# Kernel tuning notes

Measured on AMD Instinct MI355X. Metric: run time of the kernel, lower is better.

Reference implementation:

```python
import jax, jax.numpy as jnp
import numpy as np

B, T, E, QKV, H = 2, 2048, 1024, 1024, 16
DH = QKV // H
R_LAYER = 2

def rmsnorm(x):
    eps = jnp.finfo(x.dtype).eps
    return x * jax.lax.rsqrt(jnp.mean(x * x, axis=-1, keepdims=True) + eps)

def w_norm(w, n):
    # scale whole matrix so its (unbiased) std matches n**-0.5
    std = jnp.std(w, ddof=1)
    return w * (n ** -0.5 / (std + 1e-8))

def rotary(x, cos, sin):
    d = x.shape[-1] // 2
    x1, x2 = x[..., :d], x[..., d:]
    return jnp.concatenate([x1 * cos + x2 * sin, -x1 * sin + x2 * cos], axis=-1)

def w_split(w):
    w_qkv = w[:3 * QKV]                               # (3*QKV, E)
    w_sw = w[3 * QKV:5 * QKV].reshape(2 * E, QKV)     # (2*E, QKV)
    w_out = w[5 * QKV:]                               # (E, E)
    return w_qkv, w_sw, w_out

def aft(x, w_qkv):
    qkv = rmsnorm(x) @ w_qkv.T                        # (B,T,3*QKV)
    q, k, v = jnp.split(qkv, 3, axis=-1)
    q, k = rmsnorm(q), rmsnorm(k)
    wexp = jnp.exp(k)
    kv_c = jnp.cumsum(wexp * v, axis=1)
    w_c = jnp.cumsum(wexp, axis=1)
    y = jax.nn.sigmoid(q) * kv_c / (w_c + 1e-6)
    return x, y

def tea(x, cos, sin, w_qkv):
    qkv = (rmsnorm(x) @ w_qkv.T).reshape(B, T, H, 3 * DH)
    q, k, v = jnp.split(qkv, 3, axis=-1)              # each (B,T,H,DH)
    q, k = rotary(q, cos, sin), rotary(k, cos, sin)
    q, k = rmsnorm(q), rmsnorm(k)
    q = q.transpose(0, 2, 1, 3)                       # (B,H,T,DH)
    k = k.transpose(0, 2, 1, 3)
    v = v.transpose(0, 2, 1, 3)
    scores = jnp.einsum('bhqd,bhkd->bhqk', q, k) * DH ** -0.5
    mask = jnp.tril(jnp.ones((T, T), dtype=bool))
    scores = jnp.where(mask, scores, -jnp.inf)
    att = jax.nn.softmax(scores, axis=-1)
    y = jnp.einsum('bhqk,bhkd->bhqd', att, v)
    return x, y.transpose(0, 2, 1, 3).reshape(B, T, QKV)

def swiglu(x, y, w_sw, w_out, ret_oa=True):
    uv = y @ w_sw.T                                   # (B,T,2*E)
    u, v = jnp.split(uv, 2, axis=-1)
    out = x + (u * jax.nn.silu(v)) @ w_out.T
    if not ret_oa:
        return out
    o = rmsnorm(u.reshape(B * T, -1))
    a = v.reshape(B * T, -1)
    oa = jax.nn.softmax((o.T @ a) * E ** -0.5, axis=-1)  # (E,E)
    return out, oa

def setup_inputs():
    key = jax.random.key(0)
    k1, k2 = jax.random.split(key)
    x = jax.random.normal(k1, (B, T, E), dtype=jnp.float32)
    s = 3 ** 0.5 * E ** -0.5
    w = jax.random.uniform(k2, (5 * QKV + E, E), dtype=jnp.float32, minval=-s, maxval=s)
    half = DH // 2
    inv_freq = 1.0 / (10000.0 ** (jnp.arange(half, dtype=jnp.float32) / half))
    freqs = jnp.outer(jnp.arange(T, dtype=jnp.float32), inv_freq)  # (T, half)
    cos = jnp.cos(freqs)[:, None, :]                  # (T,1,half) broadcasts over (B,T,H,half)
    sin = jnp.sin(freqs)[:, None, :]
    return {"x": x, "w": w, "cos": cos, "sin": sin}

def reference(x, w, cos, sin):
    for i in range(R_LAYER):
        w_qkv, w_sw, w_out = w_split(w)
        w_qkv = w_norm(w_qkv, E)
        w_sw = w_norm(w_sw, QKV)
        w_out = w_norm(w_out, E)
        if (i + 1) % 4 == 0:
            x, y = tea(x, cos, sin, w_qkv)
        else:
            x, y = aft(x, w_qkv)
        x, oa = swiglu(x, y, w_sw, w_out, ret_oa=True)
        # RetentionMechanism.forward: hypernetwork weight mixing
        wT = w_norm(w @ oa, 5 * QKV + E)
        w = wT * jax.nn.silu(w) + w
    w_qkv, w_sw, w_out = w_split(w)                   # note: no w_norm on final split (matches source)
    x, y = tea(x, cos, sin, w_qkv)
    return swiglu(x, y, w_sw, w_out, ret_oa=False)
```

## Files before the change

kernel.cpp:

```cpp
#include <hip/hip_runtime.h>
#include <hip/hip_bf16.h>
#include <math.h>

#define TPB 256

constexpr int Bc = 2, Tc = 2048, Ec = 1024, QKVc = 1024, Hc = 16, DHc = 64;
constexpr long BT = (long)Bc * Tc;
constexpr int WR = 5 * QKVc + Ec;
constexpr float F32_EPS = 1.1920928955078125e-07f;
constexpr int NCH = 64, CHL = Tc / NCH;

typedef __attribute__((ext_vector_type(8))) short short8;
typedef __attribute__((ext_vector_type(4))) float f32x4;

__device__ __forceinline__ unsigned short f2bu(float f) {
    union { __hip_bfloat16 h; unsigned short u; } c; c.h = __float2bfloat16(f); return c.u;
}
__device__ __forceinline__ float bu2f(unsigned short u) {
    union { __hip_bfloat16 h; unsigned short u; } c; c.u = u; return __bfloat162float(c.h);
}
__device__ __forceinline__ float ldval(const float* p) { return *p; }
__device__ __forceinline__ float ldval(const unsigned short* p) { return bu2f(*p); }

__device__ __forceinline__ void gload_lds16(const void* g, void* l) {
    __builtin_amdgcn_global_load_lds((const __attribute__((address_space(1))) void*)g,
                                     (__attribute__((address_space(3))) void*)l, 16, 0, 0);
}

__global__ void k_std_partial3(const float* __restrict__ w, float* __restrict__ out) {
    __shared__ float ls[TPB], lss[TPB];
    int seg = blockIdx.y;
    long base = (seg == 0) ? 0L : (seg == 1 ? 3072L * 1024 : 5120L * 1024);
    long n    = (seg == 0) ? 3072L * 1024 : (seg == 1 ? 2048L * 1024 : 1024L * 1024);
    const float* p = w + base;
    float s = 0.f, ss = 0.f;
    for (long i = (long)blockIdx.x * TPB + threadIdx.x; i < n; i += 256L * TPB) {
        float v = p[i]; s += v; ss += v * v;
    }
    ls[threadIdx.x] = s; lss[threadIdx.x] = ss; __syncthreads();
    for (int o = 128; o > 0; o >>= 1) {
        if (threadIdx.x < o) { ls[threadIdx.x] += ls[threadIdx.x + o]; lss[threadIdx.x] += lss[threadIdx.x + o]; }
        __syncthreads();
    }
    if (threadIdx.x == 0) { out[seg * 512 + blockIdx.x] = ls[0]; out[seg * 512 + 256 + blockIdx.x] = lss[0]; }
}

__global__ void k_std_final3(const float* __restrict__ part, float* __restrict__ scales) {
    __shared__ float ls[TPB], lss[TPB];
    for (int seg = 0; seg < 3; ++seg) {
        ls[threadIdx.x] = part[seg * 512 + threadIdx.x];
        lss[threadIdx.x] = part[seg * 512 + 256 + threadIdx.x];
        __syncthreads();
        for (int o = 128; o > 0; o >>= 1) {
            if (threadIdx.x < o) { ls[threadIdx.x] += ls[threadIdx.x + o]; lss[threadIdx.x] += lss[threadIdx.x + o]; }
            __syncthreads();
        }
        if (threadIdx.x == 0) {
            float n = (seg == 0) ? 3145728.0f : (seg == 1 ? 2097152.0f : 1048576.0f);
            float var = (lss[0] - ls[0] * ls[0] / n) / (n - 1.0f);
            scales[seg] = 0.03125f / (sqrtf(fmaxf(var, 0.0f)) + 1e-8f);
        }
        __syncthreads();
    }
}

__global__ void k_std_partial(const float* __restrict__ p, long n, float* __restrict__ out) {
    __shared__ float ls[TPB], lss[TPB];
    float s = 0.f, ss = 0.f;
    for (long i = (long)blockIdx.x * TPB + threadIdx.x; i < n; i += (long)gridDim.x * TPB) {
        float v = p[i]; s += v; ss += v * v;
    }
    ls[threadIdx.x] = s; lss[threadIdx.x] = ss; __syncthreads();
    for (int o = 128; o > 0; o >>= 1) {
        if (threadIdx.x < o) { ls[threadIdx.x] += ls[threadIdx.x + o]; lss[threadIdx.x] += lss[threadIdx.x + o]; }
        __syncthreads();
    }
    if (threadIdx.x == 0) { out[blockIdx.x] = ls[0]; out[gridDim.x + blockIdx.x] = lss[0]; }
}

__global__ void k_std_final(const float* __restrict__ part, float n, float rs, float* __restrict__ scale) {
    __shared__ float ls[TPB], lss[TPB];
    ls[threadIdx.x] = part[threadIdx.x];
    lss[threadIdx.x] = part[TPB + threadIdx.x];
    __syncthreads();
    for (int o = 128; o > 0; o >>= 1) {
        if (threadIdx.x < o) { ls[threadIdx.x] += ls[threadIdx.x + o]; lss[threadIdx.x] += lss[threadIdx.x + o]; }
        __syncthreads();
    }
    if (threadIdx.x == 0) {
        float var = (lss[0] - ls[0] * ls[0] / n) / (n - 1.0f);
        scale[0] = rs / (sqrtf(fmaxf(var, 0.0f)) + 1e-8f);
    }
}

__global__ void k_rms_qk(float* __restrict__ qkv) {
    __shared__ float red[TPB];
    int bid = blockIdx.x;
    long row = bid >> 1; int half = bid & 1;
    float* p = qkv + row * 3072 + half * 1024;
    float4 v = *(const float4*)(p + threadIdx.x * 4);
    float ss = v.x * v.x + v.y * v.y + v.z * v.z + v.w * v.w;
    red[threadIdx.x] = ss; __syncthreads();
    for (int o = 128; o > 0; o >>= 1) {
        if (threadIdx.x < o) red[threadIdx.x] += red[threadIdx.x + o];
        __syncthreads();
    }
    float sc = rsqrtf(red[0] / 1024.0f + F32_EPS);
    float4 o4; o4.x = v.x * sc; o4.y = v.y * sc; o4.z = v.z * sc; o4.w = v.w * sc;
    *(float4*)(p + threadIdx.x * 4) = o4;
}

__global__ void k_rms1024b(const float* __restrict__ in, unsigned short* __restrict__ out, long ldin, long ldout) {
    __shared__ float red[TPB];
    long row = blockIdx.x;
    float4 v = *(const float4*)(in + row * ldin + threadIdx.x * 4);
    float ss = v.x * v.x + v.y * v.y + v.z * v.z + v.w * v.w;
    red[threadIdx.x] = ss; __syncthreads();
    for (int o = 128; o > 0; o >>= 1) {
        if (threadIdx.x < o) red[threadIdx.x] += red[threadIdx.x + o];
        __syncthreads();
    }
    float sc = rsqrtf(red[0] / 1024.0f + F32_EPS);
    ushort4 o4; o4.x = f2bu(v.x * sc); o4.y = f2bu(v.y * sc); o4.z = f2bu(v.z * sc); o4.w = f2bu(v.w * sc);
    *(ushort4*)(out + row * ldout + threadIdx.x * 4) = o4;
}

__global__ void k_cast_bf16(const float* __restrict__ in, unsigned short* __restrict__ out, long n4) {
    long i = (long)blockIdx.x * TPB + threadIdx.x;
    if (i >= n4) return;
    float4 v = *(const float4*)(in + i * 4);
    ushort4 o; o.x = f2bu(v.x); o.y = f2bu(v.y); o.z = f2bu(v.z); o.w = f2bu(v.w);
    *(ushort4*)(out + i * 4) = o;
}

template<typename TI>
__global__ void k_tcast(const TI* __restrict__ in, long ldi, long sIn,
                        unsigned short* __restrict__ out, long ldo, long sOut,
                        const float* __restrict__ rowscale) {
    __shared__ float tile[64][65];
    const TI* ip = in + (long)blockIdx.z * sIn;
    unsigned short* op = out + (long)blockIdx.z * sOut;
    int r0 = blockIdx.y * 64, c0 = blockIdx.x * 64;
    int tid = threadIdx.x;
    int rr = tid >> 4, cc = (tid & 15) * 4;
    #pragma unroll
    for (int u = 0; u < 4; ++u) {
        int r = rr + u * 16;
        float sc = rowscale ? rowscale[r0 + r] : 1.0f;
        #pragma unroll
        for (int j = 0; j < 4; ++j)
            tile[r][cc + j] = ldval(ip + (long)(r0 + r) * ldi + c0 + cc + j) * sc;
    }
    __syncthreads();
    #pragma unroll
    for (int u = 0; u < 4; ++u) {
        int c = rr + u * 16;
        ushort4 o;
        o.x = f2bu(tile[cc + 0][c]); o.y = f2bu(tile[cc + 1][c]);
        o.z = f2bu(tile[cc + 2][c]); o.w = f2bu(tile[cc + 3][c]);
        *(ushort4*)(op + (long)(c0 + c) * ldo + r0 + cc) = o;
    }
}

__global__ void k_tcast2(const float* __restrict__ uv, const float* __restrict__ uscale,
                         unsigned short* __restrict__ t1, unsigned short* __restrict__ t2) {
    __shared__ float tile[64][65];
    int z = blockIdx.z;
    const float* ip = uv + (z ? 1024 : 0);
    unsigned short* op = z ? t2 : t1;
    int r0 = blockIdx.y * 64, c0 = blockIdx.x * 64;
    int tid = threadIdx.x;
    int rr = tid >> 4, cc = (tid & 15) * 4;
    #pragma unroll
    for (int u = 0; u < 4; ++u) {
        int r = rr + u * 16;
        float sc = z ? 1.0f : uscale[r0 + r];
        #pragma unroll
        for (int j = 0; j < 4; ++j)
            tile[r][cc + j] = ip[(long)(r0 + r) * 2048 + c0 + cc + j] * sc;
    }
    __syncthreads();
    #pragma unroll
    for (int u = 0; u < 4; ++u) {
        int c = rr + u * 16;
        ushort4 o;
        o.x = f2bu(tile[cc + 0][c]); o.y = f2bu(tile[cc + 1][c]);
        o.z = f2bu(tile[cc + 2][c]); o.w = f2bu(tile[cc + 3][c]);
        *(ushort4*)(op + (long)(c0 + c) * 4096 + r0 + cc) = o;
    }
}

template<int WGM, int WGN, int WRITE_BF16>
__global__ __launch_bounds__(256)
void k_bgemm(int K,
             const unsigned short* __restrict__ A, int lda, long sA,
             const unsigned short* __restrict__ B, int ldb, long sB,
             void* __restrict__ C, int ldc, long sCi, long sSplit, int nsplit,
             const float* __restrict__ scale_ptr, float fscale,
             const float* __restrict__ addp, int ldadd) {
    constexpr int TM = WGM * 64, TN = WGN * 64;
    __shared__ unsigned short Asl[TM * 32];
    __shared__ unsigned short Bsl[TN * 32];
    int bz = blockIdx.z;
    int batch = bz, sp = 0;
    if (nsplit > 1) { batch = bz / nsplit; sp = bz - batch * nsplit; }
    int m0 = blockIdx.y * TM, n0 = blockIdx.x * TN;
    const unsigned short* Ap = A + (long)batch * sA + (long)sp * K;
    const unsigned short* Bp = B + (long)batch * sB + (long)sp * K;
    int tid = threadIdx.x, lane = tid & 63, wave = tid >> 6;
    int wr = wave / WGN, wc = wave % WGN;
    f32x4 acc[4][4] = {};
    constexpr int CAW = TM / 64;
    constexpr int CBW = TN / 64;
    for (int k0 = 0; k0 < K; k0 += 32) {
        #pragma unroll
        for (int c = 0; c < CAW; ++c) {
            int bu = (wave * CAW + c) * 64;
            int uidx = bu + lane;
            int r = uidx >> 2, slot = uidx & 3;
            int gu = slot ^ ((r >> 1) & 3);
            gload_lds16(Ap + (long)(m0 + r) * lda + k0 + gu * 8, Asl + bu * 8);
        }
        #pragma unroll
        for (int c = 0; c < CBW; ++c) {
            int bu = (wave * CBW + c) * 64;
            int uidx = bu + lane;
            int r = uidx >> 2, slot = uidx & 3;
            int gu = slot ^ ((r >> 1) & 3);
            gload_lds16(Bp + (long)(n0 + r) * ldb + k0 + gu * 8, Bsl + bu * 8);
        }
        __syncthreads();
        short8 av[4], bv[4];
        #pragma unroll
        for (int m = 0; m < 4; ++m) {
            int r = wr * 64 + m * 16 + (lane & 15);
            int slot = (lane >> 4) ^ ((r >> 1) & 3);
            av[m] = *(const short8*)(Asl + r * 32 + slot * 8);
        }
        #pragma unroll
        for (int n = 0; n < 4; ++n) {
            int r = wc * 64 + n * 16 + (lane & 15);
            int slot = (lane >> 4) ^ ((r >> 1) & 3);
            bv[n] = *(const short8*)(Bsl + r * 32 + slot * 8);
        }
        #pragma unroll
        for (int m = 0; m < 4; ++m)
            #pragma unroll
            for (int n = 0; n < 4; ++n)
                acc[m][n] = __builtin_amdgcn_mfma_f32_16x16x32_bf16(av[m], bv[n], acc[m][n], 0, 0, 0);
        __syncthreads();
    }
    float s = fscale * (scale_ptr ? scale_ptr[0] : 1.0f);
    long cbase = (long)batch * sCi + (long)sp * sSplit;
    int row0 = m0 + wr * 64, col0 = n0 + wc * 64 + (lane & 15);
    int rbase = (lane >> 4) * 4;
    #pragma unroll
    for (int m = 0; m < 4; ++m)
        #pragma unroll
        for (int i = 0; i < 4; ++i) {
            long row = row0 + m * 16 + rbase + i;
            #pragma unroll
            for (int n = 0; n < 4; ++n) {
                long col = col0 + n * 16;
                float v = acc[m][n][i] * s;
                if (addp) v += addp[row * (long)ldadd + col];
                long idx = cbase + row * ldc + col;
                if (WRITE_BF16) ((unsigned short*)C)[idx] = f2bu(v);
                else ((float*)C)[idx] = v;
            }
        }
}

__global__ __launch_bounds__(256)
void k_flash_split(const unsigned short* __restrict__ hq, const unsigned short* __restrict__ hk,
                   const unsigned short* __restrict__ hvT,
                   float* __restrict__ opart, float* __restrict__ mpart, float* __restrict__ lpart) {
    __shared__ unsigned short P_lds[4][32 * 72];
    int lane = threadIdx.x & 63, wave = threadIdx.x >> 6;
    unsigned short* P = P_lds[wave];
    int g = lane >> 4, c = lane & 15;
    unsigned bid = blockIdx.x;
    unsigned bswz = (bid & 7) * 160 + (bid >> 3);
    unsigned gi = bswz * 4 + wave;
    unsigned bh = gi / 160, itr = gi % 160;
    int item = 159 - (int)itr;
    int strip, chunk;
    if (item < 16)      { strip = item;                 chunk = 0; }
    else if (item < 48) { strip = 16 + (item - 16) / 2; chunk = (item - 16) & 1; }
    else if (item < 96) { strip = 32 + (item - 48) / 3; chunk = (item - 48) % 3; }
    else                { strip = 48 + (item - 96) / 4; chunk = (item - 96) & 3; }
    int q0 = strip * 32;
    int nt = (q0 + 32 + 63) >> 6;
    int ti0 = chunk * 8;
    int ti1 = ti0 + 8 < nt ? ti0 + 8 : nt;
    const unsigned short* qb = hq + (long)bh * Tc * 64;
    const unsigned short* kb = hk + (long)bh * Tc * 64;
    const unsigned short* vtb = hvT + (long)bh * 64 * Tc;

    short8 qf[2][2];
    #pragma unroll
    for (int mf = 0; mf < 2; ++mf)
        #pragma unroll
        for (int ks = 0; ks < 2; ++ks)
            qf[mf][ks] = *(const short8*)(qb + (long)(q0 + mf * 16 + c) * 64 + ks * 32 + g * 8);

    f32x4 o_acc[2][4] = {};
    float m_run[2][4], lpp[2][4];
    #pragma unroll
    for (int mf = 0; mf < 2; ++mf)
        #pragma unroll
        for (int i = 0; i < 4; ++i) { m_run[mf][i] = -3.0e38f; lpp[mf][i] = 0.f; }

    for (int ti = ti0; ti < ti1; ++ti) {
        int kt = ti * 64;
        short8 vf[2][4];
        #pragma unroll
        for (int ks = 0; ks < 2; ++ks)
            #pragma unroll
            for (int df = 0; df < 4; ++df)
                vf[ks][df] = *(const short8*)(vtb + (long)(df * 16 + c) * Tc + kt + ks * 32 + g * 8);
        f32x4 s_acc[2][4] = {};
        #pragma unroll
        for (int ks = 0; ks < 2; ++ks) {
            short8 kf[4];
            #pragma unroll
            for (int nf = 0; nf < 4; ++nf)
                kf[nf] = *(const short8*)(kb + (long)(kt + nf * 16 + c) * 64 + ks * 32 + g * 8);
            #pragma unroll
            for (int mf = 0; mf < 2; ++mf)
                #pragma unroll
                for (int nf = 0; nf < 4; ++nf)
                    s_acc[mf][nf] = __builtin_amdgcn_mfma_f32_16x16x32_bf16(qf[mf][ks], kf[nf], s_acc[mf][nf], 0, 0, 0);
        }
        if (ti == nt - 1) {
            #pragma unroll
            for (int mf = 0; mf < 2; ++mf)
                #pragma unroll
                for (int nf = 0; nf < 4; ++nf)
                    #pragma unroll
                    for (int i = 0; i < 4; ++i)
                        if ((kt + nf * 16 + c) > (q0 + mf * 16 + g * 4 + i)) s_acc[mf][nf][i] = -1.0e30f;
        }
        float pm[2][4];
        #pragma unroll
        for (int mf = 0; mf < 2; ++mf)
            #pragma unroll
            for (int i = 0; i < 4; ++i)
                pm[mf][i] = fmaxf(fmaxf(s_acc[mf][0][i], s_acc[mf][1][i]),
                                  fmaxf(s_acc[mf][2][i], s_acc[mf][3][i]));
        #pragma unroll
        for (int lvl = 1; lvl <= 8; lvl <<= 1)
            #pragma unroll
            for (int mf = 0; mf < 2; ++mf)
                #pragma unroll
                for (int i = 0; i < 4; ++i)
                    pm[mf][i] = fmaxf(pm[mf][i], __shfl_xor(pm[mf][i], lvl));
        float mg = 0.f;
        #pragma unroll
        for (int mf = 0; mf < 2; ++mf)
            #pragma unroll
            for (int i = 0; i < 4; ++i) {
                pm[mf][i] *= 0.125f;
                mg = fmaxf(mg, pm[mf][i] - m_run[mf][i]);
            }
        if (__any(mg > 8.0f)) {
            #pragma unroll
            for (int mf = 0; mf < 2; ++mf)
                #pragma unroll
                for (int i = 0; i < 4; ++i) {
                    float mn = fmaxf(m_run[mf][i], pm[mf][i]);
                    float corr = __expf(m_run[mf][i] - mn);
                    m_run[mf][i] = mn;
                    lpp[mf][i] *= corr;
                    #pragma unroll
                    for (int df = 0; df < 4; ++df) o_acc[mf][df][i] *= corr;
                }
        }
        #pragma unroll
        for (int mf = 0; mf < 2; ++mf)
            #pragma unroll
            for (int nf = 0; nf < 4; ++nf)
                #pragma unroll
                for (int i = 0; i < 4; ++i) {
                    float p = __expf(fmaf(s_acc[mf][nf][i], 0.125f, -m_run[mf][i]));
                    P[(mf * 16 + g * 4 + i) * 72 + nf * 16 + c] = f2bu(p);
                    lpp[mf][i] += p;
                }
        #pragma unroll
        for (int ks = 0; ks < 2; ++ks) {
            short8 pa[2];
            #pragma unroll
            for (int mf = 0; mf < 2; ++mf)
                pa[mf] = *(const short8*)(P + (mf * 16 + c) * 72 + ks * 32 + g * 8);
            #pragma unroll
            for (int mf = 0; mf < 2; ++mf)
                #pragma unroll
                for (int df = 0; df < 4; ++df)
                    o_acc[mf][df] = __builtin_amdgcn_mfma_f32_16x16x32_bf16(pa[mf], vf[ks][df], o_acc[mf][df], 0, 0, 0);
        }
    }
    #pragma unroll
    for (int lvl = 1; lvl <= 8; lvl <<= 1)
        #pragma unroll
        for (int mf = 0; mf < 2; ++mf)
            #pragma unroll
            for (int i = 0; i < 4; ++i)
                lpp[mf][i] += __shfl_xor(lpp[mf][i], lvl);
    long pbase = (long)(bh * 160 + item);
    #pragma unroll
    for (int mf = 0; mf < 2; ++mf)
        #pragma unroll
        for (int i = 0; i < 4; ++i) {
            int row_l = mf * 16 + g * 4 + i;
            #pragma unroll
            for (int df = 0; df < 4; ++df)
                opart[pbase * 2048 + row_l * 64 + df * 16 + c] = o_acc[mf][df][i];
            if (c == 0) {
                mpart[pbase * 32 + row_l] = m_run[mf][i];
                lpart[pbase * 32 + row_l] = lpp[mf][i];
            }
        }
}

__global__ __launch_bounds__(256)
void k_flash_merge(const float* __restrict__ opart, const float* __restrict__ mpart,
                   const float* __restrict__ lpart, unsigned short* __restrict__ yout) {
    int bs = blockIdx.x;
    int bh = bs >> 6, strip = bs & 63;
    int b = bh >> 4, h = bh & 15;
    int np, base;
    if (strip < 16)      { np = 1; base = strip; }
    else if (strip < 32) { np = 2; base = 16 + (strip - 16) * 2; }
    else if (strip < 48) { np = 3; base = 48 + (strip - 32) * 3; }
    else                 { np = 4; base = 96 + (strip - 48) * 4; }
    long p0 = (long)(bh * 160 + base);
    int tid = threadIdx.x;
    int r = tid >> 3, c0 = (tid & 7) * 8;
    float M = -3.0e38f;
    for (int p = 0; p < np; ++p) M = fmaxf(M, mpart[(p0 + p) * 32 + r]);
    float L = 0.f;
    float acc[8] = {};
    for (int p = 0; p < np; ++p) {
        float sc = __expf(mpart[(p0 + p) * 32 + r] - M);
        L += lpart[(p0 + p) * 32 + r] * sc;
        const float* op = opart + (p0 + p) * 2048 + r * 64 + c0;
        #pragma unroll
        for (int j = 0; j < 8; ++j) acc[j] += op[j] * sc;
    }
    float inv = 1.0f / L;
    long row = (long)b * Tc + strip * 32 + r;
    unsigned short* yp = yout + row * 1024 + h * 64 + c0;
    ushort4 o1, o2;
    o1.x = f2bu(acc[0] * inv); o1.y = f2bu(acc[1] * inv); o1.z = f2bu(acc[2] * inv); o1.w = f2bu(acc[3] * inv);
    o2.x = f2bu(acc[4] * inv); o2.y = f2bu(acc[5] * inv); o2.z = f2bu(acc[6] * inv); o2.w = f2bu(acc[7] * inv);
    *(ushort4*)yp = o1;
    *(ushort4*)(yp + 4) = o2;
}

__global__ void k_aft_p1(const float* __restrict__ qkv, float* __restrict__ cw, float* __restrict__ cs) {
    int id = blockIdx.x * TPB + threadIdx.x;
    int bc = id & 2047, ch = id >> 11;
    int b = bc >> 10, c = bc & 1023;
    const float* base = qkv + ((long)(b * Tc + ch * CHL)) * 3072 + c;
    float sw = 0.f, sv = 0.f;
    for (int i = 0; i < CHL; ++i) {
        float k = base[1024], v = base[2048];
        float e = __expf(k);
        sw += e; sv += e * v;
        base += 3072;
    }
    cw[ch * 2048 + bc] = sw; cs[ch * 2048 + bc] = sv;
}

__global__ void k_aft_p3(const float* __restrict__ qkv, const float* __restrict__ cw,
                         const float* __restrict__ cs, unsigned short* __restrict__ y) {
    int id = blockIdx.x * TPB + threadIdx.x;
    int bc = id & 2047, ch = id >> 11;
    int b = bc >> 10, c = bc & 1023;
    float aw = 0.f, av = 0.f;
    for (int cc = 0; cc < ch; ++cc) { aw += cw[cc * 2048 + bc]; av += cs[cc * 2048 + bc]; }
    long t0 = (long)b * Tc + ch * CHL;
    const float* base = qkv + t0 * 3072 + c;
    unsigned short* yp = y + t0 * 1024 + c;
    for (int i = 0; i < CHL; ++i) {
        float q = base[0], k = base[1024], v = base[2048];
        float e = __expf(k);
        av += e * v; aw += e;
        float sig = 1.0f / (1.0f + __expf(-q));
        yp[0] = f2bu(sig * av / (aw + 1e-6f));
        base += 3072; yp += 1024;
    }
}

__global__ void k_silu_rms(const float* __restrict__ uv, unsigned short* __restrict__ g,
                           float* __restrict__ rs) {
    __shared__ float red[TPB];
    long row = blockIdx.x;
    const float* up = uv + row * 2048;
    float4 u = *(const float4*)(up + threadIdx.x * 4);
    float4 v = *(const float4*)(up + 1024 + threadIdx.x * 4);
    ushort4 o;
    o.x = f2bu(u.x * v.x / (1.f + __expf(-v.x)));
    o.y = f2bu(u.y * v.y / (1.f + __expf(-v.y)));
    o.z = f2bu(u.z * v.z / (1.f + __expf(-v.z)));
    o.w = f2bu(u.w * v.w / (1.f + __expf(-v.w)));
    *(ushort4*)(g + row * 1024 + threadIdx.x * 4) = o;
    red[threadIdx.x] = u.x * u.x + u.y * u.y + u.z * u.z + u.w * u.w;
    __syncthreads();
    for (int off = 128; off > 0; off >>= 1) {
        if (threadIdx.x < off) red[threadIdx.x] += red[threadIdx.x + off];
        __syncthreads();
    }
    if (threadIdx.x == 0) rs[row] = rsqrtf(red[0] / 1024.0f + F32_EPS);
}

__global__ void k_silu_gate(const float* __restrict__ uv, unsigned short* __restrict__ g, long n4) {
    long i = (long)blockIdx.x * TPB + threadIdx.x;
    if (i >= n4) return;
    long r = i >> 8, c4 = i & 255;
    float4 u = *(const float4*)(uv + r * 2048 + c4 * 4);
    float4 v = *(const float4*)(uv + r * 2048 + 1024 + c4 * 4);
    ushort4 o;
    o.x = f2bu(u.x * v.x / (1.f + __expf(-v.x)));
    o.y = f2bu(u.y * v.y / (1.f + __expf(-v.y)));
    o.z = f2bu(u.z * v.z / (1.f + __expf(-v.z)));
    o.w = f2bu(u.w * v.w / (1.f + __expf(-v.w)));
    *(ushort4*)(g + r * 1024 + c4 * 4) = o;
}

__global__ void k_wupdate(float* __restrict__ wout, const float* __restrict__ win,
                          const float* __restrict__ p, const float* __restrict__ scale,
                          unsigned short* __restrict__ wb, long n4) {
    long i = (long)blockIdx.x * TPB + threadIdx.x;
    if (i >= n4) return;
    float s = scale[0];
    float4 wv = *(const float4*)(win + i * 4);
    float4 pv = *(const float4*)(p + i * 4);
    float4 o;
    o.x = pv.x * s * (wv.x / (1.f + __expf(-wv.x))) + wv.x;
    o.y = pv.y * s * (wv.y / (1.f + __expf(-wv.y))) + wv.y;
    o.z = pv.z * s * (wv.z / (1.f + __expf(-wv.z))) + wv.z;
    o.w = pv.w * s * (wv.w / (1.f + __expf(-wv.w))) + wv.w;
    *(float4*)(wout + i * 4) = o;
    ushort4 ob; ob.x = f2bu(o.x); ob.y = f2bu(o.y); ob.z = f2bu(o.z); ob.w = f2bu(o.w);
    *(ushort4*)(wb + i * 4) = ob;
}

__global__ void k_softmax4(const float* __restrict__ parts, float* __restrict__ outb, float fscale) {
    __shared__ float red[TPB];
    __shared__ float rowbuf[1024];
    long row = blockIdx.x;
    const float* p0 = parts + row * 1024;
    for (int c = threadIdx.x; c < 1024; c += TPB) {
        float v = p0[c] + p0[c + 1048576] + p0[c + 2097152] + p0[c + 3145728];
        rowbuf[c] = v * fscale;
    }
    __syncthreads();
    float m = -3.0e38f;
    for (int c = threadIdx.x; c < 1024; c += TPB) m = fmaxf(m, rowbuf[c]);
    red[threadIdx.x] = m; __syncthreads();
    for (int o = 128; o > 0; o >>= 1) {
        if (threadIdx.x < o) red[threadIdx.x] = fmaxf(red[threadIdx.x], red[threadIdx.x + o]);
        __syncthreads();
    }
    m = red[0]; __syncthreads();
    float sum = 0.f;
    for (int c = threadIdx.x; c < 1024; c += TPB) sum += __expf(rowbuf[c] - m);
    red[threadIdx.x] = sum; __syncthreads();
    for (int o = 128; o > 0; o >>= 1) {
        if (threadIdx.x < o) red[threadIdx.x] += red[threadIdx.x + o];
        __syncthreads();
    }
    float inv = 1.0f / red[0];
    for (int c = threadIdx.x; c < 1024; c += TPB)
        outb[row * 1024 + c] = __expf(rowbuf[c] - m) * inv;
}

__global__ void k_rot_split(const float* __restrict__ qkvp, const float* __restrict__ cosp,
                            const float* __restrict__ sinp, unsigned short* __restrict__ hq,
                            unsigned short* __restrict__ hk, unsigned short* __restrict__ hv) {
    __shared__ float row[3072];
    __shared__ float cs[32], sn[32];
    int bt = blockIdx.x;
    int b = bt >> 11, t = bt & 2047;
    const float* src = qkvp + (long)bt * 3072;
    #pragma unroll
    for (int u = 0; u < 3; ++u) {
        int idx = threadIdx.x + u * 256;
        *(float4*)&row[idx * 4] = *(const float4*)(src + idx * 4);
    }
    if (threadIdx.x < 32) { cs[threadIdx.x] = cosp[t * 32 + threadIdx.x]; sn[threadIdx.x] = sinp[t * 32 + threadIdx.x]; }
    __syncthreads();
    int h = threadIdx.x >> 4, li = threadIdx.x & 15;
    int base = h * 192;
    long obase = ((long)(b * Hc + h) * Tc + t) * 64 + li * 4;
    {
        float r[4]; float ss = 0.f;
        #pragma unroll
        for (int j = 0; j < 4; ++j) {
            int d = li * 4 + j;
            float val = (d < 32) ? (row[base + d] * cs[d] + row[base + d + 32] * sn[d])
                                 : (-row[base + d - 32] * sn[d - 32] + row[base + d] * cs[d - 32]);
            r[j] = val; ss += val * val;
        }
        ss += __shfl_xor(ss, 1); ss += __shfl_xor(ss, 2); ss += __shfl_xor(ss, 4); ss += __shfl_xor(ss, 8);
        float sc = rsqrtf(ss / 64.0f + F32_EPS);
        ushort4 o; o.x = f2bu(r[0] * sc); o.y = f2bu(r[1] * sc); o.z = f2bu(r[2] * sc); o.w = f2bu(r[3] * sc);
        *(ushort4*)(hq + obase) = o;
    }
    {
        int kb = base + 64;
        float r[4]; float ss = 0.f;
        #pragma unroll
        for (int j = 0; j < 4; ++j) {
            int d = li * 4 + j;
            float val = (d < 32) ? (row[kb + d] * cs[d] + row[kb + d + 32] * sn[d])
                                 : (-row[kb + d - 32] * sn[d - 32] + row[kb + d] * cs[d - 32]);
            r[j] = val; ss += val * val;
        }
        ss += __shfl_xor(ss, 1); ss += __shfl_xor(ss, 2); ss += __shfl_xor(ss, 4); ss += __shfl_xor(ss, 8);
        float sc = rsqrtf(ss / 64.0f + F32_EPS);
        ushort4 o; o.x = f2bu(r[0] * sc); o.y = f2bu(r[1] * sc); o.z = f2bu(r[2] * sc); o.w = f2bu(r[3] * sc);
        *(ushort4*)(hk + obase) = o;
    }
    {
        ushort4 o;
        o.x = f2bu(row[base + 128 + li * 4 + 0]); o.y = f2bu(row[base + 128 + li * 4 + 1]);
        o.z = f2bu(row[base + 128 + li * 4 + 2]); o.w = f2bu(row[base + 128 + li * 4 + 3]);
        *(ushort4*)(hv + obase) = o;
    }
}

extern "C" void kernel_launch(void* const* d_in, const int* in_sizes, int n_in,
                              void* d_out, int out_size, void* d_ws, size_t ws_size,
                              hipStream_t stream) {
    const float* x_in = (const float*)d_in[0];
    const float* w_in = (const float*)d_in[1];
    const float* cos_in = (const float*)d_in[2];
    const float* sin_in = (const float*)d_in[3];
    float* out = (float*)d_out;
    float* ws = (float*)d_ws;

    long off = 0;
    float* w_cur = ws + off;  off += (long)WR * Ec;
    float* w_tmp = ws + off;  off += (long)WR * Ec;
    float* xbuf  = ws + off;  off += BT * Ec;
    float* qkv   = ws + off;  off += BT * 3L * QKVc;
    float* oab   = ws + off;  off += (long)Ec * Ec;
    float* red   = ws + off;  off += 2048;
    float* scales= ws + off;  off += 16;
    float* uscale= ws + off;  off += 4096;
    float* chw   = ws + off;  off += 2048L * NCH;
    float* chs   = ws + off;  off += 2048L * NCH;
    float* uv    = qkv;
    float* opart = qkv;
    float* mpart = oab;
    float* lpart = oab + 5120L * 32;

    unsigned short* bp = (unsigned short*)(ws + off);
    long bo = 0;
    unsigned short* wb  = bp + bo; bo += (long)WR * Ec;
    unsigned short* xbn = bp + bo; bo += BT * Ec;
    unsigned short* ybn = bp + bo; bo += BT * Ec;
    unsigned short* gbn = bp + bo; bo += BT * Ec;
    unsigned short* t1  = bp + bo; bo += BT * Ec;
    unsigned short* t2  = bp + bo; bo += BT * Ec;
    unsigned short* t3  = bp + bo; bo += BT * Ec;
    unsigned short* t4  = bp + bo; bo += BT * Ec;

    const float rsWR = 1.0f / sqrtf(6144.0f);
    const long wsw = 3072L * 1024, wout = 5120L * 1024;

    k_cast_bf16<<<(int)(((long)WR * Ec / 4) / TPB), TPB, 0, stream>>>(w_in, wb, (long)WR * Ec / 4);

    for (int layer = 0; layer < 2; ++layer) {
        const float* wsrc = layer == 0 ? w_in : w_cur;
        const float* xsrc = layer == 0 ? x_in : xbuf;
        k_std_partial3<<<dim3(256, 3), TPB, 0, stream>>>(wsrc, red);
        k_std_final3<<<1, TPB, 0, stream>>>(red, scales);
        k_rms1024b<<<BT, TPB, 0, stream>>>(xsrc, xbn, 1024, 1024);
        k_bgemm<2, 2, 0><<<dim3(24, 32, 1), TPB, 0, stream>>>(
            1024, xbn, 1024, 0, wb, 1024, 0, qkv, 3072, 0, 0, 1, scales + 0, 1.0f, nullptr, 0);
        k_rms_qk<<<8192, TPB, 0, stream>>>(qkv);
        k_aft_p1<<<(2048 * NCH) / TPB, TPB, 0, stream>>>(qkv, chw, chs);
        k_aft_p3<<<(2048 * NCH) / TPB, TPB, 0, stream>>>(qkv, chw, chs, ybn);
        k_bgemm<2, 2, 0><<<dim3(16, 32, 1), TPB, 0, stream>>>(
            1024, ybn, 1024, 0, wb + wsw, 1024, 0, uv, 2048, 0, 0, 1, scales + 1, 1.0f, nullptr, 0);
        k_silu_rms<<<BT, TPB, 0, stream>>>(uv, gbn, uscale);
        k_tcast2<<<dim3(16, 64, 2), TPB, 0, stream>>>(uv, uscale, t1, t2);
        k_bgemm<2, 2, 0><<<dim3(8, 8, 4), TPB, 0, stream>>>(
            1024, t1, 4096, 0, t2, 4096, 0, w_tmp, 1024, 0, 1048576L, 4, nullptr, 1.0f, nullptr, 0);
        k_softmax4<<<1024, TPB, 0, stream>>>(w_tmp, oab, 0.03125f);
        k_tcast<float><<<dim3(16, 16, 1), TPB, 0, stream>>>(oab, 1024, 0, t3, 1024, 0, nullptr);
        k_bgemm<2, 2, 0><<<dim3(8, 32, 1), TPB, 0, stream>>>(
            1024, gbn, 1024, 0, wb + wout, 1024, 0, xbuf, 1024, 0, 0, 1, scales + 2, 1.0f, xsrc, 1024);
        k_bgemm<2, 2, 0><<<dim3(8, 48, 1), TPB, 0, stream>>>(
            1024, wb, 1024, 0, t3, 1024, 0, w_tmp, 1024, 0, 0, 1, nullptr, 1.0f, nullptr, 0);
        k_std_partial<<<256, TPB, 0, stream>>>(w_tmp, (long)WR * 1024, red);
        k_std_final<<<1, TPB, 0, stream>>>(red, (float)((long)WR * 1024), rsWR, scales + 3);
        k_wupdate<<<(int)(((long)WR * 1024 / 4) / TPB), TPB, 0, stream>>>(
            w_cur, wsrc, w_tmp, scales + 3, wb, (long)WR * 1024 / 4);
    }

    k_rms1024b<<<BT, TPB, 0, stream>>>(xbuf, xbn, 1024, 1024);
    k_bgemm<2, 2, 0><<<dim3(24, 32, 1), TPB, 0, stream>>>(
        1024, xbn, 1024, 0, wb, 1024, 0, qkv, 3072, 0, 0, 1, nullptr, 1.0f, nullptr, 0);
    k_rot_split<<<BT, TPB, 0, stream>>>(qkv, cos_in, sin_in, t1, t2, t3);
    k_tcast<unsigned short><<<dim3(1, 32, 32), TPB, 0, stream>>>(
        t3, 64, (long)Tc * 64, t4, 2048, (long)Tc * 64, nullptr);
    k_flash_split<<<dim3(1280), TPB, 0, stream>>>(t1, t2, t4, opart, mpart, lpart);
    k_flash_merge<<<dim3(2048), TPB, 0, stream>>>(opart, mpart, lpart, ybn);
    k_bgemm<2, 2, 0><<<dim3(16, 32, 1), TPB, 0, stream>>>(
        1024, ybn, 1024, 0, wb + wsw, 1024, 0, uv, 2048, 0, 0, 1, nullptr, 1.0f, nullptr, 0);
    k_silu_gate<<<(int)((BT * 1024 / 4) / TPB), TPB, 0, stream>>>(uv, gbn, BT * 1024 / 4);
    k_bgemm<2, 2, 0><<<dim3(8, 32, 1), TPB, 0, stream>>>(
        1024, gbn, 1024, 0, wb + wout, 1024, 0, out, 1024, 0, 0, 1, nullptr, 1.0f, xbuf, 1024);
}
```

Baseline: 868.3 us.

## Store QKV, UV and flash partials in bf16 and use DPP reductions

The QKV and UV GEMM outputs are now written as bf16 instead of fp32, and every consumer (rms_qk, AFT passes, silu kernels, tcast2, rot_split) reads bf16, which halves the intermediate memory traffic. Flash-attention partial outputs are also stored in bf16. Separately, the 16-lane shuffle reductions in the flash and rotary kernels are replaced with DPP-based max/sum helpers. The cost is lower precision on these intermediates, which adds rounding error before the normalizations and the cumulative sums.

Result: faster. 829.6 us (-4.5%).

```diff
diff --git a/kernel.cpp b/kernel.cpp
--- a/kernel.cpp
+++ b/kernel.cpp
@@ -25,6 +25,28 @@
 __device__ __forceinline__ void gload_lds16(const void* g, void* l) {
     __builtin_amdgcn_global_load_lds((const __attribute__((address_space(1))) void*)g,
                                      (__attribute__((address_space(3))) void*)l, 16, 0, 0);
+}
+
+template<int CTRL>
+__device__ __forceinline__ float dppf(float x) {
+    union { float f; int i; } a, b;
+    a.f = x;
+    b.i = __builtin_amdgcn_update_dpp(0, a.i, CTRL, 0xF, 0xF, true);
+    return b.f;
+}
+__device__ __forceinline__ float max16(float v) {
+    v = fmaxf(v, dppf<0xB1>(v));
+    v = fmaxf(v, dppf<0x4E>(v));
+    v = fmaxf(v, dppf<0x124>(v));
+    v = fmaxf(v, dppf<0x128>(v));
+    return v;
+}
+__device__ __forceinline__ float sum16(float v) {
+    v += dppf<0xB1>(v);
+    v += dppf<0x4E>(v);
+    v += dppf<0x124>(v);
+    v += dppf<0x128>(v);
+    return v;
 }
 
 __global__ void k_std_partial3(const float* __restrict__ w, float* __restrict__ out) {
@@ -93,21 +115,22 @@
     }
 }
 
-__global__ void k_rms_qk(float* __restrict__ qkv) {
+__global__ void k_rms_qk(unsigned short* __restrict__ qkv) {
     __shared__ float red[TPB];
     int bid = blockIdx.x;
     long row = bid >> 1; int half = bid & 1;
-    float* p = qkv + row * 3072 + half * 1024;
-    float4 v = *(const float4*)(p + threadIdx.x * 4);
-    float ss = v.x * v.x + v.y * v.y + v.z * v.z + v.w * v.w;
-    red[threadIdx.x] = ss; __syncthreads();
+    unsigned short* p = qkv + row * 3072 + half * 1024;
+    ushort4 v = *(const ushort4*)(p + threadIdx.x * 4);
+    float f0 = bu2f(v.x), f1 = bu2f(v.y), f2 = bu2f(v.z), f3 = bu2f(v.w);
+    red[threadIdx.x] = f0 * f0 + f1 * f1 + f2 * f2 + f3 * f3;
+    __syncthreads();
     for (int o = 128; o > 0; o >>= 1) {
         if (threadIdx.x < o) red[threadIdx.x] += red[threadIdx.x + o];
         __syncthreads();
     }
     float sc = rsqrtf(red[0] / 1024.0f + F32_EPS);
-    float4 o4; o4.x = v.x * sc; o4.y = v.y * sc; o4.z = v.z * sc; o4.w = v.w * sc;
-    *(float4*)(p + threadIdx.x * 4) = o4;
+    ushort4 o4; o4.x = f2bu(f0 * sc); o4.y = f2bu(f1 * sc); o4.z = f2bu(f2 * sc); o4.w = f2bu(f3 * sc);
+    *(ushort4*)(p + threadIdx.x * 4) = o4;
 }
 
 __global__ void k_rms1024b(const float* __restrict__ in, unsigned short* __restrict__ out, long ldin, long ldout) {
@@ -162,11 +185,11 @@
     }
 }
 
-__global__ void k_tcast2(const float* __restrict__ uv, const float* __restrict__ uscale,
+__global__ void k_tcast2(const unsigned short* __restrict__ uv, const float* __restrict__ uscale,
                          unsigned short* __restrict__ t1, unsigned short* __restrict__ t2) {
     __shared__ float tile[64][65];
     int z = blockIdx.z;
-    const float* ip = uv + (z ? 1024 : 0);
+    const unsigned short* ip = uv + (z ? 1024 : 0);
     unsigned short* op = z ? t2 : t1;
     int r0 = blockIdx.y * 64, c0 = blockIdx.x * 64;
     int tid = threadIdx.x;
@@ -175,9 +198,9 @@
     for (int u = 0; u < 4; ++u) {
         int r = rr + u * 16;
         float sc = z ? 1.0f : uscale[r0 + r];
-        #pragma unroll
-        for (int j = 0; j < 4; ++j)
-            tile[r][cc + j] = ip[(long)(r0 + r) * 2048 + c0 + cc + j] * sc;
+        ushort4 v = *(const ushort4*)(ip + (long)(r0 + r) * 2048 + c0 + cc);
+        tile[r][cc + 0] = bu2f(v.x) * sc; tile[r][cc + 1] = bu2f(v.y) * sc;
+        tile[r][cc + 2] = bu2f(v.z) * sc; tile[r][cc + 3] = bu2f(v.w) * sc;
     }
     __syncthreads();
     #pragma unroll
@@ -274,7 +297,7 @@
 __global__ __launch_bounds__(256)
 void k_flash_split(const unsigned short* __restrict__ hq, const unsigned short* __restrict__ hk,
                    const unsigned short* __restrict__ hvT,
-                   float* __restrict__ opart, float* __restrict__ mpart, float* __restrict__ lpart) {
+                   unsigned short* __restrict__ opart, float* __restrict__ mpart, float* __restrict__ lpart) {
     __shared__ unsigned short P_lds[4][32 * 72];
     int lane = threadIdx.x & 63, wave = threadIdx.x >> 6;
     unsigned short* P = P_lds[wave];
@@ -346,15 +369,8 @@
         for (int mf = 0; mf < 2; ++mf)
             #pragma unroll
             for (int i = 0; i < 4; ++i)
-                pm[mf][i] = fmaxf(fmaxf(s_acc[mf][0][i], s_acc[mf][1][i]),
-                                  fmaxf(s_acc[mf][2][i], s_acc[mf][3][i]));
-        #pragma unroll
-        for (int lvl = 1; lvl <= 8; lvl <<= 1)
-            #pragma unroll
-            for (int mf = 0; mf < 2; ++mf)
-                #pragma unroll
-                for (int i = 0; i < 4; ++i)
-                    pm[mf][i] = fmaxf(pm[mf][i], __shfl_xor(pm[mf][i], lvl));
+                pm[mf][i] = max16(fmaxf(fmaxf(s_acc[mf][0][i], s_acc[mf][1][i]),
+                                        fmaxf(s_acc[mf][2][i], s_acc[mf][3][i])));
         float mg = 0.f;
         #pragma unroll
         for (int mf = 0; mf < 2; ++mf)
@@ -400,12 +416,10 @@
         }
     }
     #pragma unroll
-    for (int lvl = 1; lvl <= 8; lvl <<= 1)
-        #pragma unroll
-        for (int mf = 0; mf < 2; ++mf)
-            #pragma unroll
-            for (int i = 0; i < 4; ++i)
-                lpp[mf][i] += __shfl_xor(lpp[mf][i], lvl);
+    for (int mf = 0; mf < 2; ++mf)
+        #pragma unroll
+        for (int i = 0; i < 4; ++i)
+            lpp[mf][i] = sum16(lpp[mf][i]);
     long pbase = (long)(bh * 160 + item);
     #pragma unroll
     for (int mf = 0; mf < 2; ++mf)
@@ -414,7 +428,7 @@
             int row_l = mf * 16 + g * 4 + i;
             #pragma unroll
             for (int df = 0; df < 4; ++df)
-                opart[pbase * 2048 + row_l * 64 + df * 16 + c] = o_acc[mf][df][i];
+                opart[pbase * 2048 + row_l * 64 + df * 16 + c] = f2bu(o_acc[mf][df][i]);
             if (c == 0) {
                 mpart[pbase * 32 + row_l] = m_run[mf][i];
                 lpart[pbase * 32 + row_l] = lpp[mf][i];
@@ -423,7 +437,7 @@
 }
 
 __global__ __launch_bounds__(256)
-void k_flash_merge(const float* __restrict__ opart, const float* __restrict__ mpart,
+void k_flash_merge(const unsigned short* __restrict__ opart, const float* __restrict__ mpart,
                    const float* __restrict__ lpart, unsigned short* __restrict__ yout) {
     int bs = blockIdx.x;
     int bh = bs >> 6, strip = bs & 63;
@@ -443,9 +457,13 @@
     for (int p = 0; p < np; ++p) {
         float sc = __expf(mpart[(p0 + p) * 32 + r] - M);
         L += lpart[(p0 + p) * 32 + r] * sc;
-        const float* op = opart + (p0 + p) * 2048 + r * 64 + c0;
-        #pragma unroll
-        for (int j = 0; j < 8; ++j) acc[j] += op[j] * sc;
+        const unsigned short* op = opart + (p0 + p) * 2048 + r * 64 + c0;
+        ushort4 a = *(const ushort4*)op;
+        ushort4 bq = *(const ushort4*)(op + 4);
+        acc[0] += bu2f(a.x) * sc; acc[1] += bu2f(a.y) * sc;
+        acc[2] += bu2f(a.z) * sc; acc[3] += bu2f(a.w) * sc;
+        acc[4] += bu2f(bq.x) * sc; acc[5] += bu2f(bq.y) * sc;
+        acc[6] += bu2f(bq.z) * sc; acc[7] += bu2f(bq.w) * sc;
     }
     float inv = 1.0f / L;
     long row = (long)b * Tc + strip * 32 + r;
@@ -457,14 +475,14 @@
     *(ushort4*)(yp + 4) = o2;
 }
 
-__global__ void k_aft_p1(const float* __restrict__ qkv, float* __restrict__ cw, float* __restrict__ cs) {
+__global__ void k_aft_p1(const unsigned short* __restrict__ qkv, float* __restrict__ cw, float* __restrict__ cs) {
     int id = blockIdx.x * TPB + threadIdx.x;
     int bc = id & 2047, ch = id >> 11;
     int b = bc >> 10, c = bc & 1023;
-    const float* base = qkv + ((long)(b * Tc + ch * CHL)) * 3072 + c;
+    const unsigned short* base = qkv + ((long)(b * Tc + ch * CHL)) * 3072 + c;
     float sw = 0.f, sv = 0.f;
     for (int i = 0; i < CHL; ++i) {
-        float k = base[1024], v = base[2048];
+        float k = bu2f(base[1024]), v = bu2f(base[2048]);
         float e = __expf(k);
         sw += e; sv += e * v;
         base += 3072;
@@ -472,7 +490,7 @@
     cw[ch * 2048 + bc] = sw; cs[ch * 2048 + bc] = sv;
 }
 
-__global__ void k_aft_p3(const float* __restrict__ qkv, const float* __restrict__ cw,
+__global__ void k_aft_p3(const unsigned short* __restrict__ qkv, const float* __restrict__ cw,
                          const float* __restrict__ cs, unsigned short* __restrict__ y) {
     int id = blockIdx.x * TPB + threadIdx.x;
     int bc = id & 2047, ch = id >> 11;
@@ -480,10 +498,10 @@
     float aw = 0.f, av = 0.f;
     for (int cc = 0; cc < ch; ++cc) { aw += cw[cc * 2048 + bc]; av += cs[cc * 2048 + bc]; }
     long t0 = (long)b * Tc + ch * CHL;
-    const float* base = qkv + t0 * 3072 + c;
+    const unsigned short* base = qkv + t0 * 3072 + c;
     unsigned short* yp = y + t0 * 1024 + c;
     for (int i = 0; i < CHL; ++i) {
-        float q = base[0], k = base[1024], v = base[2048];
+        float q = bu2f(base[0]), k = bu2f(base[1024]), v = bu2f(base[2048]);
         float e = __expf(k);
         av += e * v; aw += e;
         float sig = 1.0f / (1.0f + __expf(-q));
@@ -492,20 +510,22 @@
     }
 }
 
-__global__ void k_silu_rms(const float* __restrict__ uv, unsigned short* __restrict__ g,
+__global__ void k_silu_rms(const unsigned short* __restrict__ uv, unsigned short* __restrict__ g,
                            float* __restrict__ rs) {
     __shared__ float red[TPB];
     long row = blockIdx.x;
-    const float* up = uv + row * 2048;
-    float4 u = *(const float4*)(up + threadIdx.x * 4);
-    float4 v = *(const float4*)(up + 1024 + threadIdx.x * 4);
+    const unsigned short* up = uv + row * 2048;
+    ushort4 u4 = *(const ushort4*)(up + threadIdx.x * 4);
+    ushort4 v4 = *(const ushort4*)(up + 1024 + threadIdx.x * 4);
+    float u0 = bu2f(u4.x), u1 = bu2f(u4.y), u2 = bu2f(u4.z), u3 = bu2f(u4.w);
+    float v0 = bu2f(v4.x), v1 = bu2f(v4.y), v2 = bu2f(v4.z), v3 = bu2f(v4.w);
     ushort4 o;
-    o.x = f2bu(u.x * v.x / (1.f + __expf(-v.x)));
-    o.y = f2bu(u.y * v.y / (1.f + __expf(-v.y)));
-    o.z = f2bu(u.z * v.z / (1.f + __expf(-v.z)));
-    o.w = f2bu(u.w * v.w / (1.f + __expf(-v.w)));
+    o.x = f2bu(u0 * v0 / (1.f + __expf(-v0)));
+    o.y = f2bu(u1 * v1 / (1.f + __expf(-v1)));
+    o.z = f2bu(u2 * v2 / (1.f + __expf(-v2)));
+    o.w = f2bu(u3 * v3 / (1.f + __expf(-v3)));
     *(ushort4*)(g + row * 1024 + threadIdx.x * 4) = o;
-    red[threadIdx.x] = u.x * u.x + u.y * u.y + u.z * u.z + u.w * u.w;
+    red[threadIdx.x] = u0 * u0 + u1 * u1 + u2 * u2 + u3 * u3;
     __syncthreads();
     for (int off = 128; off > 0; off >>= 1) {
         if (threadIdx.x < off) red[threadIdx.x] += red[threadIdx.x + off];
@@ -514,17 +534,19 @@
     if (threadIdx.x == 0) rs[row] = rsqrtf(red[0] / 1024.0f + F32_EPS);
 }
 
-__global__ void k_silu_gate(const float* __restrict__ uv, unsigned short* __restrict__ g, long n4) {
+__global__ void k_silu_gate(const unsigned short* __restrict__ uv, unsigned short* __restrict__ g, long n4) {
     long i = (long)blockIdx.x * TPB + threadIdx.x;
     if (i >= n4) return;
     long r = i >> 8, c4 = i & 255;
-    float4 u = *(const float4*)(uv + r * 2048 + c4 * 4);
-    float4 v = *(const float4*)(uv + r * 2048 + 1024 + c4 * 4);
+    ushort4 u4 = *(const ushort4*)(uv + r * 2048 + c4 * 4);
+    ushort4 v4 = *(const ushort4*)(uv + r * 2048 + 1024 + c4 * 4);
+    float u0 = bu2f(u4.x), u1 = bu2f(u4.y), u2 = bu2f(u4.z), u3 = bu2f(u4.w);
+    float v0 = bu2f(v4.x), v1 = bu2f(v4.y), v2 = bu2f(v4.z), v3 = bu2f(v4.w);
     ushort4 o;
-    o.x = f2bu(u.x * v.x / (1.f + __expf(-v.x)));
-    o.y = f2bu(u.y * v.y / (1.f + __expf(-v.y)));
-    o.z = f2bu(u.z * v.z / (1.f + __expf(-v.z)));
-    o.w = f2bu(u.w * v.w / (1.f + __expf(-v.w)));
+    o.x = f2bu(u0 * v0 / (1.f + __expf(-v0)));
+    o.y = f2bu(u1 * v1 / (1.f + __expf(-v1)));
+    o.z = f2bu(u2 * v2 / (1.f + __expf(-v2)));
+    o.w = f2bu(u3 * v3 / (1.f + __expf(-v3)));
     *(ushort4*)(g + r * 1024 + c4 * 4) = o;
 }
 
@@ -576,18 +598,20 @@
         outb[row * 1024 + c] = __expf(rowbuf[c] - m) * inv;
 }
 
-__global__ void k_rot_split(const float* __restrict__ qkvp, const float* __restrict__ cosp,
+__global__ void k_rot_split(const unsigned short* __restrict__ qkvp, const float* __restrict__ cosp,
                             const float* __restrict__ sinp, unsigned short* __restrict__ hq,
                             unsigned short* __restrict__ hk, unsigned short* __restrict__ hv) {
     __shared__ float row[3072];
     __shared__ float cs[32], sn[32];
     int bt = blockIdx.x;
     int b = bt >> 11, t = bt & 2047;
-    const float* src = qkvp + (long)bt * 3072;
+    const unsigned short* src = qkvp + (long)bt * 3072;
     #pragma unroll
     for (int u = 0; u < 3; ++u) {
         int idx = threadIdx.x + u * 256;
-        *(float4*)&row[idx * 4] = *(const float4*)(src + idx * 4);
+        ushort4 v = *(const ushort4*)(src + idx * 4);
+        row[idx * 4 + 0] = bu2f(v.x); row[idx * 4 + 1] = bu2f(v.y);
+        row[idx * 4 + 2] = bu2f(v.z); row[idx * 4 + 3] = bu2f(v.w);
     }
     if (threadIdx.x < 32) { cs[threadIdx.x] = cosp[t * 32 + threadIdx.x]; sn[threadIdx.x] = sinp[t * 32 + threadIdx.x]; }
     __syncthreads();
@@ -603,7 +627,7 @@
                                  : (-row[base + d - 32] * sn[d - 32] + row[base + d] * cs[d - 32]);
             r[j] = val; ss += val * val;
         }
-        ss += __shfl_xor(ss, 1); ss += __shfl_xor(ss, 2); ss += __shfl_xor(ss, 4); ss += __shfl_xor(ss, 8);
+        ss = sum16(ss);
         float sc = rsqrtf(ss / 64.0f + F32_EPS);
         ushort4 o; o.x = f2bu(r[0] * sc); o.y = f2bu(r[1] * sc); o.z = f2bu(r[2] * sc); o.w = f2bu(r[3] * sc);
         *(ushort4*)(hq + obase) = o;
@@ -618,7 +642,7 @@
                                  : (-row[kb + d - 32] * sn[d - 32] + row[kb + d] * cs[d - 32]);
             r[j] = val; ss += val * val;
         }
-        ss += __shfl_xor(ss, 1); ss += __shfl_xor(ss, 2); ss += __shfl_xor(ss, 4); ss += __shfl_xor(ss, 8);
+        ss = sum16(ss);
         float sc = rsqrtf(ss / 64.0f + F32_EPS);
         ushort4 o; o.x = f2bu(r[0] * sc); o.y = f2bu(r[1] * sc); o.z = f2bu(r[2] * sc); o.w = f2bu(r[3] * sc);
         *(ushort4*)(hk + obase) = o;
@@ -645,15 +669,16 @@
     float* w_cur = ws + off;  off += (long)WR * Ec;
     float* w_tmp = ws + off;  off += (long)WR * Ec;
     float* xbuf  = ws + off;  off += BT * Ec;
-    float* qkv   = ws + off;  off += BT * 3L * QKVc;
+    float* R     = ws + off;  off += BT * 3L * QKVc;
     float* oab   = ws + off;  off += (long)Ec * Ec;
     float* red   = ws + off;  off += 2048;
     float* scales= ws + off;  off += 16;
     float* uscale= ws + off;  off += 4096;
     float* chw   = ws + off;  off += 2048L * NCH;
     float* chs   = ws + off;  off += 2048L * NCH;
-    float* uv    = qkv;
-    float* opart = qkv;
+    unsigned short* qkvb  = (unsigned short*)R;
+    unsigned short* uvb   = qkvb + 12582912L;
+    unsigned short* opartb= qkvb;
     float* mpart = oab;
     float* lpart = oab + 5120L * 32;
 
@@ -679,15 +704,15 @@
         k_std_partial3<<<dim3(256, 3), TPB, 0, stream>>>(wsrc, red);
         k_std_final3<<<1, TPB, 0, stream>>>(red, scales);
         k_rms1024b<<<BT, TPB, 0, stream>>>(xsrc, xbn, 1024, 1024);
-        k_bgemm<2, 2, 0><<<dim3(24, 32, 1), TPB, 0, stream>>>(
-            1024, xbn, 1024, 0, wb, 1024, 0, qkv, 3072, 0, 0, 1, scales + 0, 1.0f, nullptr, 0);
-        k_rms_qk<<<8192, TPB, 0, stream>>>(qkv);
-        k_aft_p1<<<(2048 * NCH) / TPB, TPB, 0, stream>>>(qkv, chw, chs);
-        k_aft_p3<<<(2048 * NCH) / TPB, TPB, 0, stream>>>(qkv, chw, chs, ybn);
-        k_bgemm<2, 2, 0><<<dim3(16, 32, 1), TPB, 0, stream>>>(
-            1024, ybn, 1024, 0, wb + wsw, 1024, 0, uv, 2048, 0, 0, 1, scales + 1, 1.0f, nullptr, 0);
-        k_silu_rms<<<BT, TPB, 0, stream>>>(uv, gbn, uscale);
-        k_tcast2<<<dim3(16, 64, 2), TPB, 0, stream>>>(uv, uscale, t1, t2);
+        k_bgemm<2, 2, 1><<<dim3(24, 32, 1), TPB, 0, stream>>>(
+            1024, xbn, 1024, 0, wb, 1024, 0, qkvb, 3072, 0, 0, 1, scales + 0, 1.0f, nullptr, 0);
+        k_rms_qk<<<8192, TPB, 0, stream>>>(qkvb);
+        k_aft_p1<<<(2048 * NCH) / TPB, TPB, 0, stream>>>(qkvb, chw, chs);
+        k_aft_p3<<<(2048 * NCH) / TPB, TPB, 0, stream>>>(qkvb, chw, chs, ybn);
+        k_bgemm<2, 2, 1><<<dim3(16, 32, 1), TPB, 0, stream>>>(
+            1024, ybn, 1024, 0, wb + wsw, 1024, 0, uvb, 2048, 0, 0, 1, scales + 1, 1.0f, nullptr, 0);
+        k_silu_rms<<<BT, TPB, 0, stream>>>(uvb, gbn, uscale);
+        k_tcast2<<<dim3(16, 64, 2), TPB, 0, stream>>>(uvb, uscale, t1, t2);
         k_bgemm<2, 2, 0><<<dim3(8, 8, 4), TPB, 0, stream>>>(
             1024, t1, 4096, 0, t2, 4096, 0, w_tmp, 1024, 0, 1048576L, 4, nullptr, 1.0f, nullptr, 0);
         k_softmax4<<<1024, TPB, 0, stream>>>(w_tmp, oab, 0.03125f);
@@ -703,16 +728,16 @@
     }
 
     k_rms1024b<<<BT, TPB, 0, stream>>>(xbuf, xbn, 1024, 1024);
-    k_bgemm<2, 2, 0><<<dim3(24, 32, 1), TPB, 0, stream>>>(
-        1024, xbn, 1024, 0, wb, 1024, 0, qkv, 3072, 0, 0, 1, nullptr, 1.0f, nullptr, 0);
-    k_rot_split<<<BT, TPB, 0, stream>>>(qkv, cos_in, sin_in, t1, t2, t3);
+    k_bgemm<2, 2, 1><<<dim3(24, 32, 1), TPB, 0, stream>>>(
+        1024, xbn, 1024, 0, wb, 1024, 0, qkvb, 3072, 0, 0, 1, nullptr, 1.0f, nullptr, 0);
+    k_rot_split<<<BT, TPB, 0, stream>>>(qkvb, cos_in, sin_in, t1, t2, t3);
     k_tcast<unsigned short><<<dim3(1, 32, 32), TPB, 0, stream>>>(
         t3, 64, (long)Tc * 64, t4, 2048, (long)Tc * 64, nullptr);
-    k_flash_split<<<dim3(1280), TPB, 0, stream>>>(t1, t2, t4, opart, mpart, lpart);
-    k_flash_merge<<<dim3(2048), TPB, 0, stream>>>(opart, mpart, lpart, ybn);
-    k_bgemm<2, 2, 0><<<dim3(16, 32, 1), TPB, 0, stream>>>(
-        1024, ybn, 1024, 0, wb + wsw, 1024, 0, uv, 2048, 0, 0, 1, nullptr, 1.0f, nullptr, 0);
-    k_silu_gate<<<(int)((BT * 1024 / 4) / TPB), TPB, 0, stream>>>(uv, gbn, BT * 1024 / 4);
+    k_flash_split<<<dim3(1280), TPB, 0, stream>>>(t1, t2, t4, opartb, mpart, lpart);
+    k_flash_merge<<<dim3(2048), TPB, 0, stream>>>(opartb, mpart, lpart, ybn);
+    k_bgemm<2, 2, 1><<<dim3(16, 32, 1), TPB, 0, stream>>>(
+        1024, ybn, 1024, 0, wb + wsw, 1024, 0, uvb, 2048, 0, 0, 1, nullptr, 1.0f, nullptr, 0);
+    k_silu_gate<<<(int)((BT * 1024 / 4) / TPB), TPB, 0, stream>>>(uvb, gbn, BT * 1024 / 4);
     k_bgemm<2, 2, 0><<<dim3(8, 32, 1), TPB, 0, stream>>>(
         1024, gbn, 1024, 0, wb + wout, 1024, 0, out, 1024, 0, 0, 1, nullptr, 1.0f, xbuf, 1024);
 }
```
